# Optimization experiments

Hardware: AMD Instinct MI355X
Metric: run time of the kernel (lower is better)

Reference implementation:

```python
import jax, jax.numpy as jnp
import numpy as np

HEADS = 4
DIM_HEAD = 32


def setup_inputs() -> dict:
    key = jax.random.key(0)
    k1, k2, k3, k4 = jax.random.split(key, 4)
    dim = 256
    hidden = HEADS * DIM_HEAD  # 128
    x = jax.random.normal(k1, (4, dim, 64, 64), dtype=jnp.float32)
    # 1x1 convs are channel-mixing matmuls; store weights as [out_ch, in_ch]
    w_qkv = jax.random.normal(k2, (3 * hidden, dim), dtype=jnp.float32) * (dim ** -0.5)
    w_out = jax.random.normal(k3, (dim, hidden), dtype=jnp.float32) * (hidden ** -0.5)
    b_out = jax.random.normal(k4, (dim,), dtype=jnp.float32) * 0.02
    return {"x": x, "w_qkv": w_qkv, "w_out": w_out, "b_out": b_out}


def reference(x, w_qkv, w_out, b_out):
    b, c, h, w = x.shape
    n = h * w
    scale = DIM_HEAD ** -0.5
    xf = x.reshape(b, c, n)                                   # b c n
    qkv = jnp.einsum('oc,bcn->bon', w_qkv, xf)                # b (3*H*D) n
    q, k, v = jnp.split(qkv, 3, axis=1)                       # each b (H*D) n
    q = q.reshape(b, HEADS, DIM_HEAD, n) * scale              # b h d n
    k = k.reshape(b, HEADS, DIM_HEAD, n)
    v = v.reshape(b, HEADS, DIM_HEAD, n)
    sim = jnp.einsum('bhdi,bhdj->bhij', q, k)                 # b h n n
    attn = jax.nn.softmax(sim, axis=-1)                       # stable max-subtract inside
    out = jnp.einsum('bhij,bhdj->bhdi', attn, v)              # b h d n
    out = out.reshape(b, HEADS * DIM_HEAD, n)                 # b (h d) n
    out = jnp.einsum('oc,bcn->bon', w_out, out) + b_out[None, :, None]
    return out.reshape(b, -1, h, w)
```

## Files before the change

kernel.cpp:

```cpp
#include <hip/hip_runtime.h>
#include <hip/hip_bf16.h>
#include <stdint.h>

#define B_SZ 4
#define C_IN 256
#define N_SP 4096
#define HEADS 4
#define DH 32
#define HID 128

#define BI 128
#define BJ 64
#define PP 68

typedef short short4v __attribute__((ext_vector_type(4)));
typedef short short8 __attribute__((ext_vector_type(8)));
typedef float f32x4 __attribute__((ext_vector_type(4)));

#if __has_builtin(__builtin_amdgcn_exp2f)
#define EXP2 __builtin_amdgcn_exp2f
#else
#define EXP2 exp2f
#endif

__device__ __forceinline__ short f2bfs(float f) {
  return (short)((__float_as_uint(f) + 0x8000u) >> 16);
}
__device__ __forceinline__ uint32_t pk_bf(float a, float b) {
  uint32_t ua = __float_as_uint(a) + 0x8000u;
  uint32_t ub = __float_as_uint(b) + 0x8000u;
  return (ua >> 16) | (ub & 0xffff0000u);
}
__device__ __forceinline__ short8 ld_frag(const short* p) {
  short4v a = *(const short4v*)p;
  short4v b = *(const short4v*)(p + 4);
  return __builtin_shufflevector(a, b, 0, 1, 2, 3, 4, 5, 6, 7);
}
__device__ __forceinline__ f32x4 mfma16(short8 a, short8 b, f32x4 c) {
  return __builtin_amdgcn_mfma_f32_16x16x32_bf16(a, b, c, 0, 0, 0);
}

__global__ __launch_bounds__(256) void qkv_proj_k(
    const float* __restrict__ x, const float* __restrict__ w,
    float* __restrict__ qkf, short* __restrict__ vt) {
  const int t = threadIdx.x;
  const int n0 = blockIdx.x * 1024 + t * 4;
  const int o0 = blockIdx.y * 8;
  const int b = blockIdx.z;
  const float* xb = x + (size_t)b * C_IN * N_SP + n0;
  float acc[8][4];
#pragma unroll
  for (int r = 0; r < 8; ++r)
#pragma unroll
    for (int j = 0; j < 4; ++j) acc[r][j] = 0.f;
  for (int c = 0; c < C_IN; c += 2) {
    const float4 xa = *(const float4*)(xb + (size_t)c * N_SP);
    const float4 xc = *(const float4*)(xb + (size_t)(c + 1) * N_SP);
    const float xaj[4] = {xa.x, xa.y, xa.z, xa.w};
    const float xcj[4] = {xc.x, xc.y, xc.z, xc.w};
#pragma unroll
    for (int r = 0; r < 8; ++r) {
      const float2 wv = *(const float2*)(w + (size_t)(o0 + r) * C_IN + c);
#pragma unroll
      for (int j = 0; j < 4; ++j) acc[r][j] += wv.x * xaj[j] + wv.y * xcj[j];
    }
  }
  if (o0 < 256) {
    float* dst = qkf + ((size_t)b * 256 + o0) * N_SP + n0;
#pragma unroll
    for (int r = 0; r < 8; ++r)
      *(float4*)(dst + (size_t)r * N_SP) =
          make_float4(acc[r][0], acc[r][1], acc[r][2], acc[r][3]);
  } else {
    const int d0 = o0 & 31, h = (o0 >> 5) & 3;
    const int bh = b * HEADS + h;
#pragma unroll
    for (int r = 0; r < 8; ++r) {
      short4v p;
#pragma unroll
      for (int j = 0; j < 4; ++j) p[j] = f2bfs(acc[r][j]);
      *(short4v*)(vt + ((size_t)bh * DH + d0 + r) * N_SP + n0) = p;
    }
  }
}

__global__ __launch_bounds__(256) void qk_t_k(
    const float* __restrict__ qkf, short* __restrict__ qt, short* __restrict__ kt) {
  __shared__ short T[256 * 36];
  const int t = threadIdx.x;
  const int ntile = blockIdx.x, bh = blockIdx.y, z = blockIdx.z;
  const int b = bh >> 2, h = bh & 3;
  const float sc = z ? 1.f : (0.17677669529663687f * 1.4426950408889634f);
  const float* src = qkf + ((size_t)(b * 256 + z * 128 + h * 32)) * N_SP + ntile * 256;
  {
    const int d = t >> 3, m = t & 7;
    const float* sp = src + (size_t)d * N_SP + m * 32;
#pragma unroll
    for (int k2 = 0; k2 < 8; ++k2) {
      const float4 v = *(const float4*)(sp + k2 * 4);
      const int n = m * 32 + k2 * 4;
      T[(n + 0) * 36 + d] = f2bfs(v.x * sc);
      T[(n + 1) * 36 + d] = f2bfs(v.y * sc);
      T[(n + 2) * 36 + d] = f2bfs(v.z * sc);
      T[(n + 3) * 36 + d] = f2bfs(v.w * sc);
    }
  }
  __syncthreads();
  short* dst = (z ? kt : qt) + ((size_t)bh * N_SP + ntile * 256) * DH;
  const int ch = t & 3, nb = t >> 2;
#pragma unroll
  for (int rep = 0; rep < 4; ++rep) {
    const int n = rep * 64 + nb;
    const uint2 a = *(const uint2*)&T[n * 36 + ch * 8];
    const uint2 c = *(const uint2*)&T[n * 36 + ch * 8 + 4];
    uint4 o; o.x = a.x; o.y = a.y; o.z = c.x; o.w = c.y;
    *(uint4*)(dst + (size_t)n * DH + ch * 8) = o;
  }
}

__global__ __launch_bounds__(256, 2) void attn_k(
    const short* __restrict__ qt, const short* __restrict__ kt,
    const short* __restrict__ vt, float* __restrict__ att) {
  __shared__ short Ps[BI * PP];
  __shared__ float Osh[DH * 132];
  const int t = threadIdx.x;
  const int lane = t & 63, w = t >> 6;
  const int l15 = lane & 15, quad = lane >> 4;
  const int i0 = blockIdx.x * BI;
  const int bh = blockIdx.y;
  const short* qg = qt + ((size_t)bh * N_SP + i0) * DH;
  const short* kg = kt + (size_t)bh * N_SP * DH;
  const short* vg = vt + (size_t)bh * DH * N_SP;

  short8 bq[2];
#pragma unroll
  for (int tt = 0; tt < 2; ++tt)
    bq[tt] = *(const short8*)(qg + (size_t)(w * 32 + tt * 16 + l15) * DH + quad * 8);

  const f32x4 zz = {0.f, 0.f, 0.f, 0.f};
  f32x4 o_acc[2][2] = {{zz, zz}, {zz, zz}};
  float lsum[2] = {0.f, 0.f};
  short* prow[2];
#pragma unroll
  for (int tt = 0; tt < 2; ++tt) prow[tt] = Ps + (w * 32 + tt * 16 + l15) * PP;

  short8 akA[4], akB[4], vbA[2][2], vbB[2][2];
#pragma unroll
  for (int jt = 0; jt < 4; ++jt)
    akA[jt] = *(const short8*)(kg + (size_t)(jt * 16 + l15) * DH + quad * 8);
#pragma unroll
  for (int dt = 0; dt < 2; ++dt)
#pragma unroll
    for (int kk = 0; kk < 2; ++kk)
      vbA[dt][kk] = *(const short8*)(vg + (size_t)(dt * 16 + l15) * N_SP + kk * 32 + quad * 8);

  auto body = [&](const short8 (&akc)[4], const short8 (&vbc)[2][2],
                  short8 (&akn)[4], short8 (&vbn)[2][2], int jn) {
    f32x4 sf[2][4];
#pragma unroll
    for (int tt = 0; tt < 2; ++tt)
#pragma unroll
      for (int jt = 0; jt < 4; ++jt) sf[tt][jt] = mfma16(akc[jt], bq[tt], zz);
#pragma unroll
    for (int jt = 0; jt < 4; ++jt)
      akn[jt] = *(const short8*)(kg + (size_t)(jn + jt * 16 + l15) * DH + quad * 8);
#pragma unroll
    for (int dt = 0; dt < 2; ++dt)
#pragma unroll
      for (int kk = 0; kk < 2; ++kk)
        vbn[dt][kk] = *(const short8*)(vg + (size_t)(dt * 16 + l15) * N_SP + jn + kk * 32 + quad * 8);
#pragma unroll
    for (int tt = 0; tt < 2; ++tt)
#pragma unroll
      for (int jt = 0; jt < 4; ++jt) {
        const float e0 = EXP2(sf[tt][jt][0]);
        const float e1 = EXP2(sf[tt][jt][1]);
        const float e2 = EXP2(sf[tt][jt][2]);
        const float e3 = EXP2(sf[tt][jt][3]);
        lsum[tt] += (e0 + e1) + (e2 + e3);
        uint2 pk; pk.x = pk_bf(e0, e1); pk.y = pk_bf(e2, e3);
        *(uint2*)(prow[tt] + jt * 16 + quad * 4) = pk;
      }
    asm volatile("s_waitcnt lgkmcnt(0)" ::: "memory");
    short8 pa[2][2];
#pragma unroll
    for (int tt = 0; tt < 2; ++tt)
#pragma unroll
      for (int kk = 0; kk < 2; ++kk) pa[tt][kk] = ld_frag(prow[tt] + kk * 32 + quad * 8);
#pragma unroll
    for (int tt = 0; tt < 2; ++tt)
#pragma unroll
      for (int dt = 0; dt < 2; ++dt) {
        o_acc[tt][dt] = mfma16(pa[tt][0], vbc[dt][0], o_acc[tt][dt]);
        o_acc[tt][dt] = mfma16(pa[tt][1], vbc[dt][1], o_acc[tt][dt]);
      }
  };

  for (int jt0 = 0; jt0 < N_SP; jt0 += 2 * BJ) {
    body(akA, vbA, akB, vbB, (jt0 + BJ) & (N_SP - 1));
    body(akB, vbB, akA, vbA, (jt0 + 2 * BJ) & (N_SP - 1));
  }

#pragma unroll
  for (int tt = 0; tt < 2; ++tt) {
    lsum[tt] += __shfl_xor(lsum[tt], 16);
    lsum[tt] += __shfl_xor(lsum[tt], 32);
  }
  float linv[2][4];
#pragma unroll
  for (int tt = 0; tt < 2; ++tt)
#pragma unroll
    for (int r = 0; r < 4; ++r) linv[tt][r] = 1.f / __shfl(lsum[tt], quad * 4 + r);
#pragma unroll
  for (int tt = 0; tt < 2; ++tt)
#pragma unroll
    for (int dt = 0; dt < 2; ++dt)
#pragma unroll
      for (int r = 0; r < 4; ++r)
        Osh[(dt * 16 + l15) * 132 + w * 32 + tt * 16 + quad * 4 + r] =
            o_acc[tt][dt][r] * linv[tt][r];
  __syncthreads();
  {
    const int d = t >> 3, ch = t & 7;
    float* dst = att + ((size_t)bh * DH + d) * N_SP + i0 + ch * 16;
    const float* src = Osh + d * 132 + ch * 16;
#pragma unroll
    for (int k2 = 0; k2 < 4; ++k2) *(float4*)(dst + k2 * 4) = *(const float4*)(src + k2 * 4);
  }
}

__global__ __launch_bounds__(256) void out_proj_k(
    const float* __restrict__ att, const float* __restrict__ w,
    const float* __restrict__ bias, float* __restrict__ out) {
  const int t = threadIdx.x;
  const int n0 = blockIdx.x * 1024 + t * 4;
  const int o0 = blockIdx.y * 8;
  const int b = blockIdx.z;
  const float* ab = att + (size_t)b * HID * N_SP + n0;
  float acc[8][4];
#pragma unroll
  for (int r = 0; r < 8; ++r)
#pragma unroll
    for (int j = 0; j < 4; ++j) acc[r][j] = 0.f;
  for (int c = 0; c < HID; c += 2) {
    const float4 a0 = *(const float4*)(ab + (size_t)c * N_SP);
    const float4 a1 = *(const float4*)(ab + (size_t)(c + 1) * N_SP);
    const float a0j[4] = {a0.x, a0.y, a0.z, a0.w};
    const float a1j[4] = {a1.x, a1.y, a1.z, a1.w};
#pragma unroll
    for (int r = 0; r < 8; ++r) {
      const float2 wv = *(const float2*)(w + (size_t)(o0 + r) * HID + c);
#pragma unroll
      for (int j = 0; j < 4; ++j) acc[r][j] += wv.x * a0j[j] + wv.y * a1j[j];
    }
  }
#pragma unroll
  for (int r = 0; r < 8; ++r) {
    const float bv = bias[o0 + r];
    *(float4*)(out + ((size_t)b * C_IN + o0 + r) * N_SP + n0) =
        make_float4(acc[r][0] + bv, acc[r][1] + bv, acc[r][2] + bv, acc[r][3] + bv);
  }
}

extern "C" void kernel_launch(void* const* d_in, const int* in_sizes, int n_in,
                              void* d_out, int out_size, void* d_ws, size_t ws_size,
                              hipStream_t stream) {
  const float* x = (const float*)d_in[0];
  const float* w_qkv = (const float*)d_in[1];
  const float* w_out = (const float*)d_in[2];
  const float* b_out = (const float*)d_in[3];
  float* out = (float*)d_out;

  short* qt = (short*)d_ws;
  short* kt = qt + (size_t)16 * N_SP * DH;
  short* vt = kt + (size_t)16 * N_SP * DH;
  float* qkf = (float*)(vt + (size_t)16 * N_SP * DH);
  float* att = qkf;

  qkv_proj_k<<<dim3(4, 48, B_SZ), 256, 0, stream>>>(x, w_qkv, qkf, vt);
  qk_t_k<<<dim3(16, 16, 2), 256, 0, stream>>>(qkf, qt, kt);
  attn_k<<<dim3(N_SP / BI, B_SZ * HEADS), 256, 0, stream>>>(qt, kt, vt, att);
  out_proj_k<<<dim3(4, 32, B_SZ), 256, 0, stream>>>(att, w_out, b_out, out);
}
```

Measured before the change: 236.9 us.

## Move QKV and output projections to split-bf16 MFMA with transposed layouts

Replaces the scalar fp32 FMA projection kernels with MFMA kernels that keep fp32 accuracy by splitting each operand into bf16 high and low parts and running three MFMAs (hi*hi, lo*hi, hi*lo). A new prep kernel transposes x to n-major and writes the hi/lo copies of x and both weight matrices. The QKV kernel now writes q/k/v directly in attention layout, so the separate transpose kernel goes away. Attention writes its output as n-major hi/lo bf16 for the output projection. The cost is extra memory traffic for the split copies and an added transpose pass.

After: 245.6 us. +3.7%, slower.

```diff
diff --git a/kernel.cpp b/kernel.cpp
--- a/kernel.cpp
+++ b/kernel.cpp
@@ -26,6 +26,9 @@
 __device__ __forceinline__ short f2bfs(float f) {
   return (short)((__float_as_uint(f) + 0x8000u) >> 16);
 }
+__device__ __forceinline__ float bfs2f(short s) {
+  return __uint_as_float(((uint32_t)(unsigned short)s) << 16);
+}
 __device__ __forceinline__ uint32_t pk_bf(float a, float b) {
   uint32_t ua = __float_as_uint(a) + 0x8000u;
   uint32_t ub = __float_as_uint(b) + 0x8000u;
@@ -40,87 +43,134 @@
   return __builtin_amdgcn_mfma_f32_16x16x32_bf16(a, b, c, 0, 0, 0);
 }
 
-__global__ __launch_bounds__(256) void qkv_proj_k(
-    const float* __restrict__ x, const float* __restrict__ w,
-    float* __restrict__ qkf, short* __restrict__ vt) {
+__global__ __launch_bounds__(256) void prep_k(
+    const float* __restrict__ x, const float* __restrict__ w_qkv,
+    const float* __restrict__ w_out,
+    short* __restrict__ xh, short* __restrict__ xl,
+    short* __restrict__ wqh, short* __restrict__ wql,
+    short* __restrict__ woh, short* __restrict__ wol) {
   const int t = threadIdx.x;
-  const int n0 = blockIdx.x * 1024 + t * 4;
-  const int o0 = blockIdx.y * 8;
-  const int b = blockIdx.z;
-  const float* xb = x + (size_t)b * C_IN * N_SP + n0;
-  float acc[8][4];
-#pragma unroll
-  for (int r = 0; r < 8; ++r)
-#pragma unroll
-    for (int j = 0; j < 4; ++j) acc[r][j] = 0.f;
-  for (int c = 0; c < C_IN; c += 2) {
-    const float4 xa = *(const float4*)(xb + (size_t)c * N_SP);
-    const float4 xc = *(const float4*)(xb + (size_t)(c + 1) * N_SP);
-    const float xaj[4] = {xa.x, xa.y, xa.z, xa.w};
-    const float xcj[4] = {xc.x, xc.y, xc.z, xc.w};
-#pragma unroll
-    for (int r = 0; r < 8; ++r) {
-      const float2 wv = *(const float2*)(w + (size_t)(o0 + r) * C_IN + c);
-#pragma unroll
-      for (int j = 0; j < 4; ++j) acc[r][j] += wv.x * xaj[j] + wv.y * xcj[j];
-    }
-  }
-  if (o0 < 256) {
-    float* dst = qkf + ((size_t)b * 256 + o0) * N_SP + n0;
-#pragma unroll
-    for (int r = 0; r < 8; ++r)
-      *(float4*)(dst + (size_t)r * N_SP) =
-          make_float4(acc[r][0], acc[r][1], acc[r][2], acc[r][3]);
+  const int bx = blockIdx.x;
+  if (bx < 256) {
+    __shared__ float T[64 * 65];
+    const int b = bx >> 6, n0 = (bx & 63) * 64;
+    const float* xb = x + (size_t)b * C_IN * N_SP;
+    for (int c0 = 0; c0 < C_IN; c0 += 64) {
+      {
+        const int n = t & 63, cw = t >> 6;
+#pragma unroll
+        for (int i = 0; i < 16; ++i) {
+          const int c = cw * 16 + i;
+          T[n * 65 + c] = xb[(size_t)(c0 + c) * N_SP + n0 + n];
+        }
+      }
+      __syncthreads();
+      {
+        const int n = t >> 2, cg = t & 3;
+#pragma unroll
+        for (int j = 0; j < 2; ++j) {
+          const int c = cg * 16 + j * 8;
+          short8 hv, lv;
+#pragma unroll
+          for (int e = 0; e < 8; ++e) {
+            const float v = T[n * 65 + c + e];
+            const short hh = f2bfs(v);
+            hv[e] = hh;
+            lv[e] = f2bfs(v - bfs2f(hh));
+          }
+          const size_t off = ((size_t)(b * N_SP + n0 + n)) * C_IN + c0 + c;
+          *(short8*)(xh + off) = hv;
+          *(short8*)(xl + off) = lv;
+        }
+      }
+      __syncthreads();
+    }
   } else {
-    const int d0 = o0 & 31, h = (o0 >> 5) & 3;
-    const int bh = b * HEADS + h;
-#pragma unroll
-    for (int r = 0; r < 8; ++r) {
+    const int f0 = (bx - 256) * 8192;
+#pragma unroll
+    for (int j = 0; j < 32; ++j) {
+      const int f = f0 + j * 256 + t;
+      float v;
+      short *dh, *dl;
+      int idx;
+      if (f < 384 * 256) { v = w_qkv[f]; dh = wqh; dl = wql; idx = f; }
+      else { idx = f - 384 * 256; v = w_out[idx]; dh = woh; dl = wol; }
+      const short hh = f2bfs(v);
+      dh[idx] = hh;
+      dl[idx] = f2bfs(v - bfs2f(hh));
+    }
+  }
+}
+
+__global__ __launch_bounds__(256) void qkv_mfma_k(
+    const short* __restrict__ xh, const short* __restrict__ xl,
+    const short* __restrict__ wqh, const short* __restrict__ wql,
+    short* __restrict__ qt, short* __restrict__ kt, short* __restrict__ vt) {
+  const int t = threadIdx.x;
+  const int lane = t & 63, w = t >> 6;
+  const int l15 = lane & 15, quad = lane >> 4;
+  const int osec = blockIdx.y, b = blockIdx.z;
+  const int n0 = blockIdx.x * 64 + w * 16;
+  const size_t xrow = ((size_t)(b * N_SP + n0 + l15)) * C_IN;
+  const size_t wrow = ((size_t)(osec * 128 + l15)) * C_IN;
+  const bool isv = (osec == 2);
+  const f32x4 zz = {0.f, 0.f, 0.f, 0.f};
+  f32x4 acc[8];
+#pragma unroll
+  for (int ot = 0; ot < 8; ++ot) acc[ot] = zz;
+
+  for (int k0 = 0; k0 < C_IN; k0 += 32) {
+    const int ko = k0 + quad * 8;
+    const short8 xhf = *(const short8*)(xh + xrow + ko);
+    const short8 xlf = *(const short8*)(xl + xrow + ko);
+#pragma unroll
+    for (int ot = 0; ot < 8; ++ot) {
+      const size_t wo = wrow + (size_t)ot * 16 * C_IN + ko;
+      const short8 whf = *(const short8*)(wqh + wo);
+      const short8 wlf = *(const short8*)(wql + wo);
+      if (isv) {
+        acc[ot] = mfma16(xhf, whf, acc[ot]);
+        acc[ot] = mfma16(xlf, whf, acc[ot]);
+        acc[ot] = mfma16(xhf, wlf, acc[ot]);
+      } else {
+        acc[ot] = mfma16(whf, xhf, acc[ot]);
+        acc[ot] = mfma16(whf, xlf, acc[ot]);
+        acc[ot] = mfma16(wlf, xhf, acc[ot]);
+      }
+    }
+  }
+
+  if (!isv) {
+    const float sc = osec ? 1.f : (0.17677669529663687f * 1.4426950408889634f);
+    short* dst = osec ? kt : qt;
+    const int n = n0 + l15;
+#pragma unroll
+    for (int ot = 0; ot < 8; ++ot) {
+      const int ol = ot * 16 + quad * 4;
+      const int h = ol >> 5, d0 = ol & 31;
       short4v p;
 #pragma unroll
-      for (int j = 0; j < 4; ++j) p[j] = f2bfs(acc[r][j]);
-      *(short4v*)(vt + ((size_t)bh * DH + d0 + r) * N_SP + n0) = p;
-    }
-  }
-}
-
-__global__ __launch_bounds__(256) void qk_t_k(
-    const float* __restrict__ qkf, short* __restrict__ qt, short* __restrict__ kt) {
-  __shared__ short T[256 * 36];
-  const int t = threadIdx.x;
-  const int ntile = blockIdx.x, bh = blockIdx.y, z = blockIdx.z;
-  const int b = bh >> 2, h = bh & 3;
-  const float sc = z ? 1.f : (0.17677669529663687f * 1.4426950408889634f);
-  const float* src = qkf + ((size_t)(b * 256 + z * 128 + h * 32)) * N_SP + ntile * 256;
-  {
-    const int d = t >> 3, m = t & 7;
-    const float* sp = src + (size_t)d * N_SP + m * 32;
-#pragma unroll
-    for (int k2 = 0; k2 < 8; ++k2) {
-      const float4 v = *(const float4*)(sp + k2 * 4);
-      const int n = m * 32 + k2 * 4;
-      T[(n + 0) * 36 + d] = f2bfs(v.x * sc);
-      T[(n + 1) * 36 + d] = f2bfs(v.y * sc);
-      T[(n + 2) * 36 + d] = f2bfs(v.z * sc);
-      T[(n + 3) * 36 + d] = f2bfs(v.w * sc);
-    }
-  }
-  __syncthreads();
-  short* dst = (z ? kt : qt) + ((size_t)bh * N_SP + ntile * 256) * DH;
-  const int ch = t & 3, nb = t >> 2;
-#pragma unroll
-  for (int rep = 0; rep < 4; ++rep) {
-    const int n = rep * 64 + nb;
-    const uint2 a = *(const uint2*)&T[n * 36 + ch * 8];
-    const uint2 c = *(const uint2*)&T[n * 36 + ch * 8 + 4];
-    uint4 o; o.x = a.x; o.y = a.y; o.z = c.x; o.w = c.y;
-    *(uint4*)(dst + (size_t)n * DH + ch * 8) = o;
+      for (int r = 0; r < 4; ++r) p[r] = f2bfs(acc[ot][r] * sc);
+      *(short4v*)(dst + ((size_t)(b * HEADS + h) * N_SP + n) * DH + d0) = p;
+    }
+  } else {
+    const int n = n0 + quad * 4;
+#pragma unroll
+    for (int ot = 0; ot < 8; ++ot) {
+      const int ol = ot * 16 + l15;
+      const int h = ol >> 5, d = ol & 31;
+      short4v p;
+#pragma unroll
+      for (int r = 0; r < 4; ++r) p[r] = f2bfs(acc[ot][r]);
+      *(short4v*)(vt + ((size_t)(b * HEADS + h) * DH + d) * N_SP + n) = p;
+    }
   }
 }
 
 __global__ __launch_bounds__(256, 2) void attn_k(
     const short* __restrict__ qt, const short* __restrict__ kt,
-    const short* __restrict__ vt, float* __restrict__ att) {
+    const short* __restrict__ vt, short* __restrict__ ath,
+    short* __restrict__ atl) {
   __shared__ short Ps[BI * PP];
   __shared__ float Osh[DH * 132];
   const int t = threadIdx.x;
@@ -221,44 +271,64 @@
             o_acc[tt][dt][r] * linv[tt][r];
   __syncthreads();
   {
-    const int d = t >> 3, ch = t & 7;
-    float* dst = att + ((size_t)bh * DH + d) * N_SP + i0 + ch * 16;
-    const float* src = Osh + d * 132 + ch * 16;
-#pragma unroll
-    for (int k2 = 0; k2 < 4; ++k2) *(float4*)(dst + k2 * 4) = *(const float4*)(src + k2 * 4);
-  }
-}
-
-__global__ __launch_bounds__(256) void out_proj_k(
-    const float* __restrict__ att, const float* __restrict__ w,
+    const int ii = t & 127, half = t >> 7;
+    const int b = bh >> 2, h = bh & 3;
+#pragma unroll
+    for (int j = 0; j < 2; ++j) {
+      short8 hv, lv;
+#pragma unroll
+      for (int e = 0; e < 8; ++e) {
+        const int d = half * 16 + j * 8 + e;
+        const float v = Osh[d * 132 + ii];
+        const short hh = f2bfs(v);
+        hv[e] = hh;
+        lv[e] = f2bfs(v - bfs2f(hh));
+      }
+      const size_t off =
+          ((size_t)(b * N_SP + i0 + ii)) * HID + h * 32 + half * 16 + j * 8;
+      *(short8*)(ath + off) = hv;
+      *(short8*)(atl + off) = lv;
+    }
+  }
+}
+
+__global__ __launch_bounds__(256) void out_mfma_k(
+    const short* __restrict__ ath, const short* __restrict__ atl,
+    const short* __restrict__ woh, const short* __restrict__ wol,
     const float* __restrict__ bias, float* __restrict__ out) {
   const int t = threadIdx.x;
-  const int n0 = blockIdx.x * 1024 + t * 4;
-  const int o0 = blockIdx.y * 8;
-  const int b = blockIdx.z;
-  const float* ab = att + (size_t)b * HID * N_SP + n0;
-  float acc[8][4];
-#pragma unroll
-  for (int r = 0; r < 8; ++r)
-#pragma unroll
-    for (int j = 0; j < 4; ++j) acc[r][j] = 0.f;
-  for (int c = 0; c < HID; c += 2) {
-    const float4 a0 = *(const float4*)(ab + (size_t)c * N_SP);
-    const float4 a1 = *(const float4*)(ab + (size_t)(c + 1) * N_SP);
-    const float a0j[4] = {a0.x, a0.y, a0.z, a0.w};
-    const float a1j[4] = {a1.x, a1.y, a1.z, a1.w};
-#pragma unroll
-    for (int r = 0; r < 8; ++r) {
-      const float2 wv = *(const float2*)(w + (size_t)(o0 + r) * HID + c);
-#pragma unroll
-      for (int j = 0; j < 4; ++j) acc[r][j] += wv.x * a0j[j] + wv.y * a1j[j];
-    }
-  }
-#pragma unroll
-  for (int r = 0; r < 8; ++r) {
-    const float bv = bias[o0 + r];
-    *(float4*)(out + ((size_t)b * C_IN + o0 + r) * N_SP + n0) =
-        make_float4(acc[r][0] + bv, acc[r][1] + bv, acc[r][2] + bv, acc[r][3] + bv);
+  const int lane = t & 63, w = t >> 6;
+  const int l15 = lane & 15, quad = lane >> 4;
+  const int osec = blockIdx.y, b = blockIdx.z;
+  const int n0 = blockIdx.x * 64 + w * 16;
+  const size_t arow = ((size_t)(b * N_SP + n0 + l15)) * HID;
+  const size_t wrow = ((size_t)(osec * 128 + l15)) * HID;
+  const f32x4 zz = {0.f, 0.f, 0.f, 0.f};
+  f32x4 acc[8];
+#pragma unroll
+  for (int ot = 0; ot < 8; ++ot) acc[ot] = zz;
+
+  for (int k0 = 0; k0 < HID; k0 += 32) {
+    const int ko = k0 + quad * 8;
+    const short8 ahf = *(const short8*)(ath + arow + ko);
+    const short8 alf = *(const short8*)(atl + arow + ko);
+#pragma unroll
+    for (int ot = 0; ot < 8; ++ot) {
+      const size_t wo = wrow + (size_t)ot * 16 * HID + ko;
+      const short8 whf = *(const short8*)(woh + wo);
+      const short8 wlf = *(const short8*)(wol + wo);
+      acc[ot] = mfma16(ahf, whf, acc[ot]);
+      acc[ot] = mfma16(alf, whf, acc[ot]);
+      acc[ot] = mfma16(ahf, wlf, acc[ot]);
+    }
+  }
+#pragma unroll
+  for (int ot = 0; ot < 8; ++ot) {
+    const int o = osec * 128 + ot * 16 + l15;
+    const float bv = bias[o];
+    float4 v = make_float4(acc[ot][0] + bv, acc[ot][1] + bv,
+                           acc[ot][2] + bv, acc[ot][3] + bv);
+    *(float4*)(out + ((size_t)(b * C_IN + o)) * N_SP + n0 + quad * 4) = v;
   }
 }
 
@@ -271,14 +341,20 @@
   const float* b_out = (const float*)d_in[3];
   float* out = (float*)d_out;
 
-  short* qt = (short*)d_ws;
+  short* xh = (short*)d_ws;
+  short* xl = xh + (size_t)B_SZ * N_SP * C_IN;
+  short* wqh = xl + (size_t)B_SZ * N_SP * C_IN;
+  short* wql = wqh + 384 * C_IN;
+  short* woh = wql + 384 * C_IN;
+  short* wol = woh + C_IN * HID;
+  short* qt = wol + C_IN * HID;
   short* kt = qt + (size_t)16 * N_SP * DH;
   short* vt = kt + (size_t)16 * N_SP * DH;
-  float* qkf = (float*)(vt + (size_t)16 * N_SP * DH);
-  float* att = qkf;
-
-  qkv_proj_k<<<dim3(4, 48, B_SZ), 256, 0, stream>>>(x, w_qkv, qkf, vt);
-  qk_t_k<<<dim3(16, 16, 2), 256, 0, stream>>>(qkf, qt, kt);
-  attn_k<<<dim3(N_SP / BI, B_SZ * HEADS), 256, 0, stream>>>(qt, kt, vt, att);
-  out_proj_k<<<dim3(4, 32, B_SZ), 256, 0, stream>>>(att, w_out, b_out, out);
-}
+  short* ath = xh;
+  short* atl = ath + (size_t)B_SZ * N_SP * HID;
+
+  prep_k<<<dim3(272), 256, 0, stream>>>(x, w_qkv, w_out, xh, xl, wqh, wql, woh, wol);
+  qkv_mfma_k<<<dim3(64, 3, B_SZ), 256, 0, stream>>>(xh, xl, wqh, wql, qt, kt, vt);
+  attn_k<<<dim3(N_SP / BI, B_SZ * HEADS), 256, 0, stream>>>(qt, kt, vt, ath, atl);
+  out_mfma_k<<<dim3(64, 2, B_SZ), 256, 0, stream>>>(ath, atl, woh, wol, b_out, out);
+}
```
